# Optimization experiments

Measured on AMD Instinct MI355X. Metric: run time of the kernel, lower is better.

Reference implementation:

```python
import jax, jax.numpy as jnp
import numpy as np

INPUT_SIZE = 1024
HIDDEN_SIZE = 1024
BATCH = 16384


def setup_inputs() -> dict:
    key = jax.random.key(0)
    kx, kh, kw, kb = jax.random.split(key, 4)
    x = jax.random.normal(kx, (BATCH, INPUT_SIZE), dtype=jnp.float32)
    hidden = jax.random.normal(kh, (BATCH, HIDDEN_SIZE), dtype=jnp.float32)
    fan_in = INPUT_SIZE + HIDDEN_SIZE
    bound = 1.0 / np.sqrt(fan_in)
    # torch Linear: weight [out, in], bias [out], uniform(-bound, bound)
    W = jax.random.uniform(kw, (HIDDEN_SIZE, fan_in), minval=-bound, maxval=bound, dtype=jnp.float32)
    b = jax.random.uniform(kb, (HIDDEN_SIZE,), minval=-bound, maxval=bound, dtype=jnp.float32)
    return {"x": x, "hidden": hidden, "W": W, "b": b}


def reference(x, hidden, W, b):
    # Batched equivalent of the per-sample loop: concat features, linear, tanh.
    xh = jnp.concatenate([x, hidden], axis=1)            # [B, in+hid]
    return jnp.tanh(xh @ W.T + b)                        # [B, hid]
```

## Files before the change

### kernel.cpp

```cpp
#include <hip/hip_runtime.h>
#include <hip/hip_bf16.h>


typedef __bf16 bf16_t;
typedef __bf16 bf16x8 __attribute__((ext_vector_type(8)));
typedef float  f32x4  __attribute__((ext_vector_type(4)));

#define M_GLOBAL 16384
#define N_GLOBAL 1024
#define K_GLOBAL 2048
#define IN_STRIDE 1024
#define NT 32

__device__ __forceinline__ float fast_tanh(float v) {
    float e = __expf(2.0f * v);
    return 1.0f - 2.0f * __builtin_amdgcn_rcpf(e + 1.0f);
}

#define W_UNITS ((long long)N_GLOBAL * K_GLOBAL / 8)

__global__ __launch_bounds__(256)
void cvt_w(const float* __restrict__ W, bf16_t* __restrict__ Wb)
{
    for (long long u = (long long)blockIdx.x * 256 + threadIdx.x; u < W_UNITS;
         u += (long long)gridDim.x * 256) {
        const long long e = u * 8;
        const float4 v0 = *(const float4*)(W + e);
        const float4 v1 = *(const float4*)(W + e + 4);
        bf16x8 o;
        o[0] = (bf16_t)v0.x; o[1] = (bf16_t)v0.y;
        o[2] = (bf16_t)v0.z; o[3] = (bf16_t)v0.w;
        o[4] = (bf16_t)v1.x; o[5] = (bf16_t)v1.y;
        o[6] = (bf16_t)v1.z; o[7] = (bf16_t)v1.w;
        *(bf16x8*)(Wb + e) = o;
    }
}

__device__ __forceinline__ void gload_lds16(const bf16_t* g, bf16_t* l) {
    __builtin_amdgcn_global_load_lds(
        (const __attribute__((address_space(1))) void*)g,
        (__attribute__((address_space(3))) void*)l, 16, 0, 0);
}

__global__ __launch_bounds__(1024)
void gemm_fa(const float* __restrict__ x, const float* __restrict__ h,
             const bf16_t* __restrict__ Wb,
             const float* __restrict__ bias, float* __restrict__ out)
{
    __shared__ __align__(16) bf16_t lds[2 * 32768];

    const int tid = threadIdx.x;
    const int xx = blockIdx.x & 7;
    const int gg = blockIdx.x >> 3;
    const int bm = (xx * 8 + (gg & 7)) * 256;
    const int bn = (gg >> 3) * 256;

    const int lane = tid & 63;
    const int wid  = tid >> 6;
    const int wm = wid >> 2;
    const int wn = wid & 3;
    const int lr = lane & 15;
    const int lk = lane >> 4;
    const int s7 = lr & 7;

    const int srow = lane >> 3;
    const int q8   = lane & 7;

    const int arow0 = bm + wid * 8 + srow;
    const bf16_t* bS = Wb + (size_t)(bn + wid * 8 + srow) * K_GLOBAL
                          + (q8 ^ srow) * 8;

    const int aWr = wid * 512 + srow * 64 + (q8 ^ srow) * 8;

    const int aRd = (wm >> 1) * 8192 + ((wm & 1) * 64 + lr) * 64;
    const int bRd = (2 + (wn >> 1)) * 8192 + ((wn & 1) * 64 + lr) * 64;

    f32x4 acc[4][4];
#pragma unroll
    for (int i = 0; i < 4; ++i)
#pragma unroll
        for (int j = 0; j < 4; ++j)
            acc[i][j] = (f32x4){0.f, 0.f, 0.f, 0.f};

    float4 ar[2][2];

#define LOAD_A(T) {                                                           \
    const int k0_ = (T) * 64;                                                 \
    const float* s_ = (k0_ < 1024) ? (x + k0_) : (h + (k0_ - 1024));          \
    _Pragma("unroll")                                                         \
    for (int p_ = 0; p_ < 2; ++p_) {                                          \
        const float* r_ = s_ + (size_t)(arow0 + p_ * 128) * IN_STRIDE + q8 * 8; \
        ar[p_][0] = *(const float4*)(r_);                                     \
        ar[p_][1] = *(const float4*)(r_ + 4);                                 \
    }                                                                         \
}

#define CVT_WRITE_A(D) {                                                      \
    _Pragma("unroll")                                                         \
    for (int p_ = 0; p_ < 2; ++p_) {                                          \
        bf16x8 v_;                                                            \
        v_[0] = (bf16_t)ar[p_][0].x; v_[1] = (bf16_t)ar[p_][0].y;             \
        v_[2] = (bf16_t)ar[p_][0].z; v_[3] = (bf16_t)ar[p_][0].w;             \
        v_[4] = (bf16_t)ar[p_][1].x; v_[5] = (bf16_t)ar[p_][1].y;             \
        v_[6] = (bf16_t)ar[p_][1].z; v_[7] = (bf16_t)ar[p_][1].w;             \
        *(bf16x8*)(lds + (D) * 32768 + p_ * 8192 + aWr) = v_;                 \
    }                                                                         \
}

#define STAGE_B(T, D) {                                                       \
    _Pragma("unroll")                                                         \
    for (int p_ = 2; p_ < 4; ++p_) {                                          \
        gload_lds16(bS + (size_t)((p_ & 1) * 128) * K_GLOBAL + (T) * 64,      \
                    lds + (D) * 32768 + p_ * 8192 + wid * 512);               \
    }                                                                         \
}

#define BAR() { asm volatile("" ::: "memory");                                \
                __builtin_amdgcn_s_barrier();                                 \
                asm volatile("" ::: "memory"); }
#define VM0()   asm volatile("s_waitcnt vmcnt(0)" ::: "memory")
#define LGKM0() asm volatile("s_waitcnt lgkmcnt(0)" ::: "memory")

    LOAD_A(0);
    STAGE_B(0, 0);
    VM0();
    CVT_WRITE_A(0);
    LGKM0();
    BAR();

    for (int t = 0; t < NT; ++t) {
        const bf16_t* lb = lds + (t & 1) * 32768;

        if (t + 1 < NT) { LOAD_A(t + 1); STAGE_B(t + 1, (t + 1) & 1); }

        __builtin_amdgcn_s_setprio(1);
#pragma unroll
        for (int kk = 0; kk < 2; ++kk) {
            const int sl = ((kk * 4 + lk) ^ s7) * 8;
            bf16x8 bq[4];
#pragma unroll
            for (int nf = 0; nf < 4; ++nf)
                bq[nf] = *(const bf16x8*)(lb + bRd + nf * 1024 + sl);
#pragma unroll
            for (int mf = 0; mf < 4; ++mf) {
                bf16x8 af = *(const bf16x8*)(lb + aRd + mf * 1024 + sl);
#pragma unroll
                for (int nf = 0; nf < 4; ++nf)
                    acc[mf][nf] = __builtin_amdgcn_mfma_f32_16x16x32_bf16(
                        af, bq[nf], acc[mf][nf], 0, 0, 0);
            }
        }
        __builtin_amdgcn_s_setprio(0);

        if (t + 1 < NT) {
            VM0();
            CVT_WRITE_A((t + 1) & 1);
            LGKM0();
            BAR();
        }
    }

#undef LOAD_A
#undef CVT_WRITE_A
#undef STAGE_B
#undef BAR
#undef VM0
#undef LGKM0

    float bv[4];
#pragma unroll
    for (int nf = 0; nf < 4; ++nf)
        bv[nf] = bias[bn + wn * 64 + nf * 16 + lr];
#pragma unroll
    for (int mf = 0; mf < 4; ++mf) {
#pragma unroll
        for (int nf = 0; nf < 4; ++nf) {
            const int col = bn + wn * 64 + nf * 16 + lr;
#pragma unroll
            for (int r = 0; r < 4; ++r) {
                const int row = bm + wm * 64 + mf * 16 + lk * 4 + r;
                out[(size_t)row * N_GLOBAL + col] = fast_tanh(acc[mf][nf][r] + bv[nf]);
            }
        }
    }
}

#define FNT 32
__global__ __launch_bounds__(256, 2)
void rnncell_fused(const float* __restrict__ x, const float* __restrict__ h,
                   const float* __restrict__ W, const float* __restrict__ bias,
                   float* __restrict__ out)
{
    __shared__ __align__(16) bf16_t As[2][128 * 64];
    __shared__ __align__(16) bf16_t Bs[2][128 * 64];

    const int tid = threadIdx.x;
    const int bid = blockIdx.x;
    const int bm = (bid >> 3) * 128;
    const int bn = (bid & 7) * 128;

    const int lane = tid & 63;
    const int wid  = tid >> 6;
    const int wr = (wid >> 1) * 64;
    const int wc = (wid & 1) * 64;
    const int lr = lane & 15;
    const int lk = lane >> 4;

    const int row0 = tid >> 3;
    const int sl0  = tid & 7;

    f32x4 acc[4][4];
#pragma unroll
    for (int i = 0; i < 4; ++i)
#pragma unroll
        for (int j = 0; j < 4; ++j)
            acc[i][j] = (f32x4){0.f, 0.f, 0.f, 0.f};

    float4 la[4][2], lb[4][2];

#define F_LOAD_A(T) do {                                                      \
    const int k0_ = (T) * 64;                                                 \
    const float* sA_ = (k0_ < 1024)                                           \
        ? (x + (size_t)bm * IN_STRIDE + k0_)                                  \
        : (h + (size_t)bm * IN_STRIDE + (k0_ - 1024));                        \
    _Pragma("unroll")                                                         \
    for (int i_ = 0; i_ < 4; ++i_) {                                          \
        const float* pa_ = sA_ + (size_t)(row0 + i_ * 32) * IN_STRIDE + sl0 * 8; \
        la[i_][0] = *(const float4*)(pa_);                                    \
        la[i_][1] = *(const float4*)(pa_ + 4);                                \
    }                                                                         \
} while (0)

#define F_LOAD_B(T) do {                                                      \
    const float* sB_ = W + (size_t)bn * K_GLOBAL + (T) * 64;                  \
    _Pragma("unroll")                                                         \
    for (int i_ = 0; i_ < 4; ++i_) {                                          \
        const float* pb_ = sB_ + (size_t)(row0 + i_ * 32) * K_GLOBAL + sl0 * 8; \
        lb[i_][0] = *(const float4*)(pb_);                                    \
        lb[i_][1] = *(const float4*)(pb_ + 4);                                \
    }                                                                         \
} while (0)

    F_LOAD_A(0);
    F_LOAD_B(0);

    for (int t = 0; t < FNT; ++t) {
        bf16_t* __restrict__ Ab = As[t & 1];
        bf16_t* __restrict__ Bb = Bs[t & 1];

#pragma unroll
        for (int i = 0; i < 4; ++i) {
            const int row = row0 + i * 32;
            const int ssl = sl0 ^ (row & 7);
            bf16x8 va;
            va[0] = (bf16_t)la[i][0].x; va[1] = (bf16_t)la[i][0].y;
            va[2] = (bf16_t)la[i][0].z; va[3] = (bf16_t)la[i][0].w;
            va[4] = (bf16_t)la[i][1].x; va[5] = (bf16_t)la[i][1].y;
            va[6] = (bf16_t)la[i][1].z; va[7] = (bf16_t)la[i][1].w;
            *(bf16x8*)(Ab + row * 64 + ssl * 8) = va;
        }
#pragma unroll
        for (int i = 0; i < 4; ++i) {
            const int row = row0 + i * 32;
            const int ssl = sl0 ^ (row & 7);
            bf16x8 vb;
            vb[0] = (bf16_t)lb[i][0].x; vb[1] = (bf16_t)lb[i][0].y;
            vb[2] = (bf16_t)lb[i][0].z; vb[3] = (bf16_t)lb[i][0].w;
            vb[4] = (bf16_t)lb[i][1].x; vb[5] = (bf16_t)lb[i][1].y;
            vb[6] = (bf16_t)lb[i][1].z; vb[7] = (bf16_t)lb[i][1].w;
            *(bf16x8*)(Bb + row * 64 + ssl * 8) = vb;
        }

        __syncthreads();

        if (t + 1 < FNT) F_LOAD_A(t + 1);

#pragma unroll
        for (int kk = 0; kk < 2; ++kk) {
            bf16x8 af[4], bfr[4];
#pragma unroll
            for (int mf = 0; mf < 4; ++mf) {
                const int row = wr + mf * 16 + lr;
                const int sl  = (kk * 4 + lk) ^ (row & 7);
                af[mf] = *(const bf16x8*)(Ab + row * 64 + sl * 8);
            }
#pragma unroll
            for (int nf = 0; nf < 4; ++nf) {
                const int row = wc + nf * 16 + lr;
                const int sl  = (kk * 4 + lk) ^ (row & 7);
                bfr[nf] = *(const bf16x8*)(Bb + row * 64 + sl * 8);
            }
#pragma unroll
            for (int mf = 0; mf < 4; ++mf)
#pragma unroll
                for (int nf = 0; nf < 4; ++nf)
                    acc[mf][nf] = __builtin_amdgcn_mfma_f32_16x16x32_bf16(
                        af[mf], bfr[nf], acc[mf][nf], 0, 0, 0);
        }

        if (t + 1 < FNT) F_LOAD_B(t + 1);
    }
#undef F_LOAD_A
#undef F_LOAD_B

    float bv[4];
#pragma unroll
    for (int nf = 0; nf < 4; ++nf)
        bv[nf] = bias[bn + wc + nf * 16 + lr];
#pragma unroll
    for (int mf = 0; mf < 4; ++mf) {
#pragma unroll
        for (int nf = 0; nf < 4; ++nf) {
            const int col = bn + wc + nf * 16 + lr;
#pragma unroll
            for (int r = 0; r < 4; ++r) {
                const int row = bm + wr + mf * 16 + lk * 4 + r;
                out[(size_t)row * N_GLOBAL + col] = fast_tanh(acc[mf][nf][r] + bv[nf]);
            }
        }
    }
}

extern "C" void kernel_launch(void* const* d_in, const int* in_sizes, int n_in,
                              void* d_out, int out_size, void* d_ws, size_t ws_size,
                              hipStream_t stream) {
    (void)in_sizes; (void)n_in; (void)out_size;
    const float* x = (const float*)d_in[0];
    const float* h = (const float*)d_in[1];
    const float* W = (const float*)d_in[2];
    const float* b = (const float*)d_in[3];
    float* out = (float*)d_out;

    const size_t need = (size_t)N_GLOBAL * K_GLOBAL * sizeof(bf16_t);
    if (ws_size >= need) {
        bf16_t* Wb = (bf16_t*)d_ws;
        cvt_w<<<512, 256, 0, stream>>>(W, Wb);
        gemm_fa<<<256, 1024, 0, stream>>>(x, h, Wb, b, out);
    } else {
        rnncell_fused<<<1024, 256, 0, stream>>>(x, h, W, b, out);
    }
}
```

Measured before the change: 85.36 us.

## Shrink GEMM block to 256x128 with K-step 32 for two blocks per CU

Replaces the 1024-thread, 256x256-tile GEMM with a 512-thread kernel on 256x128 tiles and a K step of 32, launching 512 blocks instead of 256. LDS per block drops from 128KB to 48KB, so two blocks can share a CU and hide each other's barrier and load stalls. The cost is twice as many K iterations and barriers, more A re-reads (A is loaded once per N tile), and a new XOR swizzle for the narrower LDS rows.

Result: slower. 98.27 us (+15.1%).

```diff
diff --git a/kernel.cpp b/kernel.cpp
--- a/kernel.cpp
+++ b/kernel.cpp
@@ -10,7 +10,7 @@
 #define N_GLOBAL 1024
 #define K_GLOBAL 2048
 #define IN_STRIDE 1024
-#define NT 32
+#define NT 64
 
 __device__ __forceinline__ float fast_tanh(float v) {
     float e = __expf(2.0f * v);
@@ -42,38 +42,37 @@
         (__attribute__((address_space(3))) void*)l, 16, 0, 0);
 }
 
-__global__ __launch_bounds__(1024)
-void gemm_fa(const float* __restrict__ x, const float* __restrict__ h,
+__global__ __launch_bounds__(512)
+void gemm_2b(const float* __restrict__ x, const float* __restrict__ h,
              const bf16_t* __restrict__ Wb,
              const float* __restrict__ bias, float* __restrict__ out)
 {
-    __shared__ __align__(16) bf16_t lds[2 * 32768];
+    __shared__ __align__(16) bf16_t lds[2 * 12288];
 
     const int tid = threadIdx.x;
     const int xx = blockIdx.x & 7;
-    const int gg = blockIdx.x >> 3;
-    const int bm = (xx * 8 + (gg & 7)) * 256;
-    const int bn = (gg >> 3) * 256;
+    const int jj = blockIdx.x >> 3;
+    const int bm = (xx * 8 + (jj & 7)) * 256;
+    const int bn = (jj >> 3) * 128;
 
     const int lane = tid & 63;
     const int wid  = tid >> 6;
-    const int wm = wid >> 2;
-    const int wn = wid & 3;
+    const int wm = wid >> 1;
+    const int wn = wid & 1;
     const int lr = lane & 15;
     const int lk = lane >> 4;
-    const int s7 = lr & 7;
-
-    const int srow = lane >> 3;
-    const int q8   = lane & 7;
-
-    const int arow0 = bm + wid * 8 + srow;
-    const bf16_t* bS = Wb + (size_t)(bn + wid * 8 + srow) * K_GLOBAL
-                          + (q8 ^ srow) * 8;
-
-    const int aWr = wid * 512 + srow * 64 + (q8 ^ srow) * 8;
-
-    const int aRd = (wm >> 1) * 8192 + ((wm & 1) * 64 + lr) * 64;
-    const int bRd = (2 + (wn >> 1)) * 8192 + ((wn & 1) * 64 + lr) * 64;
+    const int s3 = lr & 3;
+
+    const int sr16 = lane >> 2;
+    const int q4   = lane & 3;
+    const int arow0 = bm + wid * 16 + sr16;
+    const bf16_t* bS = Wb + (size_t)(bn + wid * 16 + sr16) * K_GLOBAL
+                          + ((q4 ^ (sr16 & 3)) * 8);
+    const int aWr = (wid * 16 + sr16) * 32 + ((q4 ^ (sr16 & 3)) * 8);
+
+    const int aRd = (wm * 64 + lr) * 32;
+    const int bRd = 8192 + (wn * 64 + lr) * 32;
+    const int sl  = ((lk ^ s3) * 8);
 
     f32x4 acc[4][4];
 #pragma unroll
@@ -85,11 +84,11 @@
     float4 ar[2][2];
 
 #define LOAD_A(T) {                                                           \
-    const int k0_ = (T) * 64;                                                 \
+    const int k0_ = (T) * 32;                                                 \
     const float* s_ = (k0_ < 1024) ? (x + k0_) : (h + (k0_ - 1024));          \
     _Pragma("unroll")                                                         \
     for (int p_ = 0; p_ < 2; ++p_) {                                          \
-        const float* r_ = s_ + (size_t)(arow0 + p_ * 128) * IN_STRIDE + q8 * 8; \
+        const float* r_ = s_ + (size_t)(arow0 + p_ * 128) * IN_STRIDE + q4 * 8; \
         ar[p_][0] = *(const float4*)(r_);                                     \
         ar[p_][1] = *(const float4*)(r_ + 4);                                 \
     }                                                                         \
@@ -103,16 +102,13 @@
         v_[2] = (bf16_t)ar[p_][0].z; v_[3] = (bf16_t)ar[p_][0].w;             \
         v_[4] = (bf16_t)ar[p_][1].x; v_[5] = (bf16_t)ar[p_][1].y;             \
         v_[6] = (bf16_t)ar[p_][1].z; v_[7] = (bf16_t)ar[p_][1].w;             \
-        *(bf16x8*)(lds + (D) * 32768 + p_ * 8192 + aWr) = v_;                 \
+        *(bf16x8*)(lds + (D) * 12288 + p_ * 4096 + aWr) = v_;                 \
     }                                                                         \
 }
 
 #define STAGE_B(T, D) {                                                       \
-    _Pragma("unroll")                                                         \
-    for (int p_ = 2; p_ < 4; ++p_) {                                          \
-        gload_lds16(bS + (size_t)((p_ & 1) * 128) * K_GLOBAL + (T) * 64,      \
-                    lds + (D) * 32768 + p_ * 8192 + wid * 512);               \
-    }                                                                         \
+    gload_lds16(bS + (size_t)(T) * 32,                                        \
+                lds + (D) * 12288 + 8192 + wid * 512);                        \
 }
 
 #define BAR() { asm volatile("" ::: "memory");                                \
@@ -129,21 +125,19 @@
     BAR();
 
     for (int t = 0; t < NT; ++t) {
-        const bf16_t* lb = lds + (t & 1) * 32768;
+        const bf16_t* lb = lds + (t & 1) * 12288;
 
         if (t + 1 < NT) { LOAD_A(t + 1); STAGE_B(t + 1, (t + 1) & 1); }
 
         __builtin_amdgcn_s_setprio(1);
-#pragma unroll
-        for (int kk = 0; kk < 2; ++kk) {
-            const int sl = ((kk * 4 + lk) ^ s7) * 8;
+        {
             bf16x8 bq[4];
 #pragma unroll
             for (int nf = 0; nf < 4; ++nf)
-                bq[nf] = *(const bf16x8*)(lb + bRd + nf * 1024 + sl);
+                bq[nf] = *(const bf16x8*)(lb + bRd + nf * 512 + sl);
 #pragma unroll
             for (int mf = 0; mf < 4; ++mf) {
-                bf16x8 af = *(const bf16x8*)(lb + aRd + mf * 1024 + sl);
+                bf16x8 af = *(const bf16x8*)(lb + aRd + mf * 512 + sl);
 #pragma unroll
                 for (int nf = 0; nf < 4; ++nf)
                     acc[mf][nf] = __builtin_amdgcn_mfma_f32_16x16x32_bf16(
@@ -335,7 +329,7 @@
     if (ws_size >= need) {
         bf16_t* Wb = (bf16_t*)d_ws;
         cvt_w<<<512, 256, 0, stream>>>(W, Wb);
-        gemm_fa<<<256, 1024, 0, stream>>>(x, h, Wb, b, out);
+        gemm_2b<<<512, 512, 0, stream>>>(x, h, Wb, b, out);
     } else {
         rnncell_fused<<<1024, 256, 0, stream>>>(x, h, W, b, out);
     }
```
